# Kernel optimization log

Hardware: AMD Instinct MI355X
Metric: run time of the kernel (lower is better)

The kernel has to match this reference:

```python
import jax, jax.numpy as jnp
import numpy as np

N = 1_000_000
D_IN = 57   # hardcoded reshape(1,57) in original aggregate()
D_OUT = 128
K = 3       # num_sample=3 hardcoded in _get_unique_neighs_list


def _masked_mean_aggregate(h, neigh_idx, neigh_mask):
    # h: [N, D]; neigh_idx: [N, K] int; neigh_mask: [N, K] {0,1}
    feats = h[neigh_idx]                                   # [N, K, D] gather
    m = neigh_mask.astype(h.dtype)[..., None]              # [N, K, 1]
    s = jnp.sum(feats * m, axis=1)                         # [N, D]
    cnt = jnp.maximum(jnp.sum(neigh_mask, axis=1, keepdims=True).astype(h.dtype), 1.0)
    return s / cnt                                         # mask.mm(embed_matrix) equivalent (segment mean)


def _sage_layer(self_feats, aggregate_feats, W):
    # combined = cat([self, agg], dim=1); relu(W @ combined^T)^T; L2 normalize
    combined = jnp.concatenate([self_feats, aggregate_feats], axis=1)  # [N, 2D]
    out = jax.nn.relu(combined @ W.T)                                  # [N, out]
    norm = jnp.linalg.norm(out, axis=-1, keepdims=True)
    return out / jnp.maximum(norm, 1e-12)                              # F.normalize p=2 eps=1e-12


def setup_inputs() -> dict:
    key = jax.random.key(0)
    ks = jax.random.split(key, 7)
    x = jax.random.normal(ks[0], (N, D_IN), dtype=jnp.float32)
    W1 = jax.random.normal(ks[1], (D_OUT, 2 * D_IN), dtype=jnp.float32) * 0.1
    W2 = jax.random.normal(ks[2], (D_OUT, 2 * D_OUT), dtype=jnp.float32) * 0.1
    neigh_idx1 = jax.random.randint(ks[3], (N, K), 0, N, dtype=jnp.int32)
    neigh_mask1 = jax.random.randint(ks[4], (N, K), 0, 2, dtype=jnp.int32)
    neigh_idx2 = jax.random.randint(ks[5], (N, K), 0, N, dtype=jnp.int32)
    neigh_mask2 = jax.random.randint(ks[6], (N, K), 0, 2, dtype=jnp.int32)
    return {"x": x, "W1": W1, "W2": W2,
            "neigh_idx1": neigh_idx1, "neigh_mask1": neigh_mask1,
            "neigh_idx2": neigh_idx2, "neigh_mask2": neigh_mask2}


def reference(x, W1, W2, neigh_idx1, neigh_mask1, neigh_idx2, neigh_mask2):
    # Layer 1: aggregate over sampled neighbors of raw features, then SageLayer
    agg1 = _masked_mean_aggregate(x, neigh_idx1, neigh_mask1)
    h1 = _sage_layer(x, agg1, W1)                 # [N, D_OUT]
    # Layer 2
    agg2 = _masked_mean_aggregate(h1, neigh_idx2, neigh_mask2)
    h2 = _sage_layer(h1, agg2, W2)                # [N, D_OUT]
    return h2
```

## Files before the change

### kernel.cpp

```cpp
#include <hip/hip_runtime.h>
#include <hip/hip_bf16.h>

#define NN 1000000
#define NG 15625

typedef short bf16x8 __attribute__((ext_vector_type(8)));
typedef float f32x4  __attribute__((ext_vector_type(4)));
typedef unsigned short u16x8 __attribute__((ext_vector_type(8)));
typedef unsigned short u16x4 __attribute__((ext_vector_type(4)));

__device__ __forceinline__ float bf2f(unsigned short u){
  unsigned int x = ((unsigned int)u) << 16; float f;
  __builtin_memcpy(&f, &x, 4); return f;
}
__device__ __forceinline__ short f2bf(float v){
  __hip_bfloat16 h = __float2bfloat16(v); short s;
  __builtin_memcpy(&s, &h, 2); return s;
}

__global__ __launch_bounds__(256, 2) void sage2_mfma(
    const unsigned short* __restrict__ h1, const float* __restrict__ W2,
    const int* __restrict__ nidx, const int* __restrict__ nmask,
    float* __restrict__ out)
{
  __shared__ unsigned short comb[64 * 256];
  __shared__ float red[64][4];
  const int t   = threadIdx.x;
  const int l   = t & 63;
  const int w   = t >> 6;
  const int cfr = l & 15;
  const int kg  = l >> 4;

  bf16x8 Bf[8][2];
  #pragma unroll
  for (int ks = 0; ks < 8; ++ks) {
    #pragma unroll
    for (int nf = 0; nf < 2; ++nf) {
      const int col = w*32 + nf*16 + cfr;
      const int k0  = ks*32 + kg*8;
      const float* p = W2 + col*256 + k0;
      f32x4 a = *reinterpret_cast<const f32x4*>(p);
      f32x4 b = *reinterpret_cast<const f32x4*>(p + 4);
      bf16x8 v;
      v[0]=f2bf(a[0]); v[1]=f2bf(a[1]); v[2]=f2bf(a[2]); v[3]=f2bf(a[3]);
      v[4]=f2bf(b[0]); v[5]=f2bf(b[1]); v[6]=f2bf(b[2]); v[7]=f2bf(b[3]);
      Bf[ks][nf] = v;
    }
  }

  const u16x8* hp = reinterpret_cast<const u16x8*>(h1);
  char* cb = reinterpret_cast<char*>(comb);

  u16x8 sS[4], s0[4], s1[4], s2[4];
  float m0[4], m1[4], m2[4], iv[4];

  auto ISSUE = [&](int g){
    const long gb = (long)g * 64;
    #pragma unroll
    for (int i = 0; i < 4; ++i) {
      int it = t + i*256;
      int n = it >> 4, q = it & 15;
      long node = gb + n;
      int j0 = nidx[node*3+0], j1 = nidx[node*3+1], j2 = nidx[node*3+2];
      int b0 = nmask[node*3+0], b1 = nmask[node*3+1], b2 = nmask[node*3+2];
      m0[i]=(float)b0; m1[i]=(float)b1; m2[i]=(float)b2;
      int c = b0+b1+b2; iv[i] = 1.0f/(float)(c<1?1:c);
      u16x8 z = {};
      sS[i] = hp[node*16 + q];
      s0[i] = b0 ? hp[(long)j0*16 + q] : z;
      s1[i] = b1 ? hp[(long)j1*16 + q] : z;
      s2[i] = b2 ? hp[(long)j2*16 + q] : z;
    }
  };

  if (blockIdx.x < NG) ISSUE(blockIdx.x);

  for (int g = blockIdx.x; g < NG; g += gridDim.x) {
    const long gb = (long)g * 64;
    #pragma unroll
    for (int i = 0; i < 4; ++i) {
      int it = t + i*256;
      int n = it >> 4, q = it & 15;
      int sw = (n & 7) << 4;
      *reinterpret_cast<u16x8*>(cb + n*512 + ((q*16) ^ sw)) = sS[i];
      u16x8 r;
      #pragma unroll
      for (int j = 0; j < 8; ++j)
        r[j] = (unsigned short)f2bf(
            (m0[i]*bf2f(s0[i][j]) + m1[i]*bf2f(s1[i][j]) + m2[i]*bf2f(s2[i][j])) * iv[i]);
      *reinterpret_cast<u16x8*>(cb + n*512 + ((256 + q*16) ^ sw)) = r;
    }
    __syncthreads();

    int gn = g + gridDim.x;
    if (gn < NG) ISSUE(gn);

    f32x4 acc[4][2];
    #pragma unroll
    for (int r = 0; r < 4; ++r) {
      acc[r][0] = (f32x4){0.f,0.f,0.f,0.f};
      acc[r][1] = (f32x4){0.f,0.f,0.f,0.f};
    }
    const int sw = (cfr & 7) << 4;
    #pragma unroll
    for (int r = 0; r < 4; ++r) {
      const int rb = (r*16 + cfr) * 512;
      #pragma unroll
      for (int ks = 0; ks < 8; ++ks) {
        bf16x8 af = *reinterpret_cast<const bf16x8*>(cb + rb + ((ks*64 + kg*16) ^ sw));
        acc[r][0] = __builtin_amdgcn_mfma_f32_16x16x32_bf16(af, Bf[ks][0], acc[r][0], 0,0,0);
        acc[r][1] = __builtin_amdgcn_mfma_f32_16x16x32_bf16(af, Bf[ks][1], acc[r][1], 0,0,0);
      }
    }

    float ssv[4][4];
    #pragma unroll
    for (int r = 0; r < 4; ++r) {
      #pragma unroll
      for (int e = 0; e < 4; ++e) {
        float v0 = fmaxf(acc[r][0][e], 0.f); acc[r][0][e] = v0;
        float v1 = fmaxf(acc[r][1][e], 0.f); acc[r][1][e] = v1;
        float s = v0*v0 + v1*v1;
        s += __shfl_xor(s, 1); s += __shfl_xor(s, 2);
        s += __shfl_xor(s, 4); s += __shfl_xor(s, 8);
        ssv[r][e] = s;
      }
      if (cfr < 4) {
        float v = cfr==0 ? ssv[r][0] : cfr==1 ? ssv[r][1] : cfr==2 ? ssv[r][2] : ssv[r][3];
        red[r*16 + kg*4 + cfr][w] = v;
      }
    }
    __syncthreads();

    #pragma unroll
    for (int r = 0; r < 4; ++r) {
      #pragma unroll
      for (int e = 0; e < 4; ++e) {
        int row = r*16 + kg*4 + e;
        float tot = red[row][0] + red[row][1] + red[row][2] + red[row][3];
        float inv = 1.0f / fmaxf(sqrtf(tot), 1e-12f);
        long node = gb + row;
        out[node*128 + w*32 + cfr]      = acc[r][0][e] * inv;
        out[node*128 + w*32 + 16 + cfr] = acc[r][1][e] * inv;
      }
    }
  }
}

__global__ __launch_bounds__(256, 2) void sage1_mfma(
    const float* __restrict__ x, const float* __restrict__ W1,
    const int* __restrict__ nidx, const int* __restrict__ nmask,
    unsigned short* __restrict__ h1)
{
  __shared__ unsigned short comb[64 * 128];
  __shared__ float red[64][4];
  const int t   = threadIdx.x;
  const int l   = t & 63;
  const int w   = t >> 6;
  const int cfr = l & 15;
  const int kg  = l >> 4;

  bf16x8 Bf[4][2];
  #pragma unroll
  for (int ks = 0; ks < 4; ++ks) {
    #pragma unroll
    for (int nf = 0; nf < 2; ++nf) {
      const int col = w*32 + nf*16 + cfr;
      const int k0  = ks*32 + kg*8;
      bf16x8 v;
      #pragma unroll
      for (int j = 0; j < 8; ++j) {
        int lk = k0 + j;
        int wk = lk < 64 ? lk : lk - 7;
        bool valid = (lk < 57) || (lk >= 64 && lk < 121);
        v[j] = valid ? f2bf(W1[col*114 + wk]) : (short)0;
      }
      Bf[ks][nf] = v;
    }
  }

  char* cb = reinterpret_cast<char*>(comb);

  f32x4 sf[4], n0[4], n1[4], n2[4];
  float m0[4], m1[4], m2[4], iv[4];

  auto ISSUE = [&](int g){
    const long gb = (long)g * 64;
    #pragma unroll
    for (int i = 0; i < 4; ++i) {
      int it = t + i*256;
      int n = it >> 4, q = it & 15;
      long node = gb + n;
      int j0 = nidx[node*3+0], j1 = nidx[node*3+1], j2 = nidx[node*3+2];
      int b0 = nmask[node*3+0], b1 = nmask[node*3+1], b2 = nmask[node*3+2];
      m0[i]=(float)b0; m1[i]=(float)b1; m2[i]=(float)b2;
      int c = b0+b1+b2; iv[i] = 1.0f/(float)(c<1?1:c);
      #pragma unroll
      for (int jj = 0; jj < 4; ++jj) {
        int j = q*4 + jj;
        bool jv = j < 57;
        sf[i][jj] = jv            ? x[node*57 + j]       : 0.f;
        n0[i][jj] = (b0 && jv)    ? x[(long)j0*57 + j]   : 0.f;
        n1[i][jj] = (b1 && jv)    ? x[(long)j1*57 + j]   : 0.f;
        n2[i][jj] = (b2 && jv)    ? x[(long)j2*57 + j]   : 0.f;
      }
    }
  };

  if (blockIdx.x < NG) ISSUE(blockIdx.x);

  for (int g = blockIdx.x; g < NG; g += gridDim.x) {
    const long gb = (long)g * 64;
    #pragma unroll
    for (int i = 0; i < 4; ++i) {
      int it = t + i*256;
      int n = it >> 4, q = it & 15;
      int sw = (n & 7) << 4;
      u16x4 vs, va;
      #pragma unroll
      for (int jj = 0; jj < 4; ++jj) {
        vs[jj] = (unsigned short)f2bf(sf[i][jj]);
        va[jj] = (unsigned short)f2bf(
            (m0[i]*n0[i][jj] + m1[i]*n1[i][jj] + m2[i]*n2[i][jj]) * iv[i]);
      }
      *reinterpret_cast<u16x4*>(cb + n*256 + ((q*8) ^ sw))        = vs;
      *reinterpret_cast<u16x4*>(cb + n*256 + ((128 + q*8) ^ sw))  = va;
    }
    __syncthreads();

    int gn = g + gridDim.x;
    if (gn < NG) ISSUE(gn);

    f32x4 acc[4][2];
    #pragma unroll
    for (int r = 0; r < 4; ++r) {
      acc[r][0] = (f32x4){0.f,0.f,0.f,0.f};
      acc[r][1] = (f32x4){0.f,0.f,0.f,0.f};
    }
    const int sw = (cfr & 7) << 4;
    #pragma unroll
    for (int r = 0; r < 4; ++r) {
      const int rb = (r*16 + cfr) * 256;
      #pragma unroll
      for (int ks = 0; ks < 4; ++ks) {
        bf16x8 af = *reinterpret_cast<const bf16x8*>(cb + rb + ((ks*64 + kg*16) ^ sw));
        acc[r][0] = __builtin_amdgcn_mfma_f32_16x16x32_bf16(af, Bf[ks][0], acc[r][0], 0,0,0);
        acc[r][1] = __builtin_amdgcn_mfma_f32_16x16x32_bf16(af, Bf[ks][1], acc[r][1], 0,0,0);
      }
    }

    float ssv[4][4];
    #pragma unroll
    for (int r = 0; r < 4; ++r) {
      #pragma unroll
      for (int e = 0; e < 4; ++e) {
        float v0 = fmaxf(acc[r][0][e], 0.f); acc[r][0][e] = v0;
        float v1 = fmaxf(acc[r][1][e], 0.f); acc[r][1][e] = v1;
        float s = v0*v0 + v1*v1;
        s += __shfl_xor(s, 1); s += __shfl_xor(s, 2);
        s += __shfl_xor(s, 4); s += __shfl_xor(s, 8);
        ssv[r][e] = s;
      }
      if (cfr < 4) {
        float v = cfr==0 ? ssv[r][0] : cfr==1 ? ssv[r][1] : cfr==2 ? ssv[r][2] : ssv[r][3];
        red[r*16 + kg*4 + cfr][w] = v;
      }
    }
    __syncthreads();

    #pragma unroll
    for (int r = 0; r < 4; ++r) {
      #pragma unroll
      for (int e = 0; e < 4; ++e) {
        int row = r*16 + kg*4 + e;
        float tot = red[row][0] + red[row][1] + red[row][2] + red[row][3];
        float inv = 1.0f / fmaxf(sqrtf(tot), 1e-12f);
        long node = gb + row;
        h1[node*128 + w*32 + cfr]      = (unsigned short)f2bf(acc[r][0][e] * inv);
        h1[node*128 + w*32 + 16 + cfr] = (unsigned short)f2bf(acc[r][1][e] * inv);
      }
    }
  }
}

extern "C" void kernel_launch(void* const* d_in, const int* in_sizes, int n_in,
                              void* d_out, int out_size, void* d_ws, size_t ws_size,
                              hipStream_t stream) {
  const float* x   = (const float*)d_in[0];
  const float* W1  = (const float*)d_in[1];
  const float* W2  = (const float*)d_in[2];
  const int* idx1  = (const int*)d_in[3];
  const int* msk1  = (const int*)d_in[4];
  const int* idx2  = (const int*)d_in[5];
  const int* msk2  = (const int*)d_in[6];
  float* out = (float*)d_out;
  unsigned short* h1 = (unsigned short*)d_ws;

  sage1_mfma<<<2048, 256, 0, stream>>>(x, W1, idx1, msk1, h1);
  sage2_mfma<<<1024, 256, 0, stream>>>(h1, W2, idx2, msk2, out);
}
```

Baseline: 735.7 us.

## Use 512-thread blocks with double-buffered LDS and two-stage index/gather prefetch

```diff
diff --git a/kernel.cpp b/kernel.cpp
--- a/kernel.cpp
+++ b/kernel.cpp
@@ -3,6 +3,7 @@
 
 #define NN 1000000
 #define NG 15625
+#define GRID 1024
 
 typedef short bf16x8 __attribute__((ext_vector_type(8)));
 typedef float f32x4  __attribute__((ext_vector_type(4)));
@@ -18,68 +19,70 @@
   __builtin_memcpy(&s, &h, 2); return s;
 }
 
-__global__ __launch_bounds__(256, 2) void sage2_mfma(
+__global__ __launch_bounds__(512, 4) void sage2_mfma(
     const unsigned short* __restrict__ h1, const float* __restrict__ W2,
     const int* __restrict__ nidx, const int* __restrict__ nmask,
     float* __restrict__ out)
 {
-  __shared__ unsigned short comb[64 * 256];
-  __shared__ float red[64][4];
+  __shared__ unsigned short comb[2][64 * 256];
+  __shared__ float red[64][8];
   const int t   = threadIdx.x;
   const int l   = t & 63;
   const int w   = t >> 6;
   const int cfr = l & 15;
   const int kg  = l >> 4;
 
-  bf16x8 Bf[8][2];
+  bf16x8 Bf[8];
   #pragma unroll
   for (int ks = 0; ks < 8; ++ks) {
-    #pragma unroll
-    for (int nf = 0; nf < 2; ++nf) {
-      const int col = w*32 + nf*16 + cfr;
-      const int k0  = ks*32 + kg*8;
-      const float* p = W2 + col*256 + k0;
-      f32x4 a = *reinterpret_cast<const f32x4*>(p);
-      f32x4 b = *reinterpret_cast<const f32x4*>(p + 4);
-      bf16x8 v;
-      v[0]=f2bf(a[0]); v[1]=f2bf(a[1]); v[2]=f2bf(a[2]); v[3]=f2bf(a[3]);
-      v[4]=f2bf(b[0]); v[5]=f2bf(b[1]); v[6]=f2bf(b[2]); v[7]=f2bf(b[3]);
-      Bf[ks][nf] = v;
-    }
+    const int col = w*16 + cfr;
+    const int k0  = ks*32 + kg*8;
+    const float* p = W2 + col*256 + k0;
+    f32x4 a = *reinterpret_cast<const f32x4*>(p);
+    f32x4 b = *reinterpret_cast<const f32x4*>(p + 4);
+    bf16x8 v;
+    v[0]=f2bf(a[0]); v[1]=f2bf(a[1]); v[2]=f2bf(a[2]); v[3]=f2bf(a[3]);
+    v[4]=f2bf(b[0]); v[5]=f2bf(b[1]); v[6]=f2bf(b[2]); v[7]=f2bf(b[3]);
+    Bf[ks] = v;
   }
 
   const u16x8* hp = reinterpret_cast<const u16x8*>(h1);
-  char* cb = reinterpret_cast<char*>(comb);
-
-  u16x8 sS[4], s0[4], s1[4], s2[4];
-  float m0[4], m1[4], m2[4], iv[4];
-
-  auto ISSUE = [&](int g){
-    const long gb = (long)g * 64;
-    #pragma unroll
-    for (int i = 0; i < 4; ++i) {
-      int it = t + i*256;
+
+  int nib0[2], nib1[2], nib2[2], nmb0[2], nmb1[2], nmb2[2];
+  u16x8 sS[2], s0[2], s1[2], s2[2];
+  float m0[2], m1[2], m2[2], iv[2];
+
+  auto IDX = [&](int g){
+    const long gb = (long)g * 64;
+    #pragma unroll
+    for (int i = 0; i < 2; ++i) {
+      int n = (t + i*512) >> 4;
+      long node = gb + n;
+      nib0[i] = nidx[node*3+0]; nib1[i] = nidx[node*3+1]; nib2[i] = nidx[node*3+2];
+      nmb0[i] = nmask[node*3+0]; nmb1[i] = nmask[node*3+1]; nmb2[i] = nmask[node*3+2];
+    }
+  };
+  auto GATHER = [&](int g){
+    const long gb = (long)g * 64;
+    #pragma unroll
+    for (int i = 0; i < 2; ++i) {
+      int it = t + i*512;
       int n = it >> 4, q = it & 15;
       long node = gb + n;
-      int j0 = nidx[node*3+0], j1 = nidx[node*3+1], j2 = nidx[node*3+2];
-      int b0 = nmask[node*3+0], b1 = nmask[node*3+1], b2 = nmask[node*3+2];
+      int b0 = nmb0[i], b1 = nmb1[i], b2 = nmb2[i];
       m0[i]=(float)b0; m1[i]=(float)b1; m2[i]=(float)b2;
       int c = b0+b1+b2; iv[i] = 1.0f/(float)(c<1?1:c);
-      u16x8 z = {};
       sS[i] = hp[node*16 + q];
-      s0[i] = b0 ? hp[(long)j0*16 + q] : z;
-      s1[i] = b1 ? hp[(long)j1*16 + q] : z;
-      s2[i] = b2 ? hp[(long)j2*16 + q] : z;
-    }
-  };
-
-  if (blockIdx.x < NG) ISSUE(blockIdx.x);
-
-  for (int g = blockIdx.x; g < NG; g += gridDim.x) {
-    const long gb = (long)g * 64;
-    #pragma unroll
-    for (int i = 0; i < 4; ++i) {
-      int it = t + i*256;
+      s0[i] = hp[(long)nib0[i]*16 + q];
+      s1[i] = hp[(long)nib1[i]*16 + q];
+      s2[i] = hp[(long)nib2[i]*16 + q];
+    }
+  };
+  auto UNPACK = [&](int p){
+    char* cb = reinterpret_cast<char*>(comb[p]);
+    #pragma unroll
+    for (int i = 0; i < 2; ++i) {
+      int it = t + i*512;
       int n = it >> 4, q = it & 15;
       int sw = (n & 7) << 4;
       *reinterpret_cast<u16x8*>(cb + n*512 + ((q*16) ^ sw)) = sS[i];
@@ -90,26 +93,34 @@
             (m0[i]*bf2f(s0[i][j]) + m1[i]*bf2f(s1[i][j]) + m2[i]*bf2f(s2[i][j])) * iv[i]);
       *reinterpret_cast<u16x8*>(cb + n*512 + ((256 + q*16) ^ sw)) = r;
     }
+  };
+
+  const int g0 = blockIdx.x;
+  IDX(g0); GATHER(g0);
+  if (g0 + (int)gridDim.x < NG) IDX(g0 + gridDim.x);
+
+  int p = 0;
+  for (int g = g0; g < NG; g += gridDim.x) {
+    const long gb = (long)g * 64;
+    UNPACK(p);
     __syncthreads();
 
-    int gn = g + gridDim.x;
-    if (gn < NG) ISSUE(gn);
-
-    f32x4 acc[4][2];
-    #pragma unroll
-    for (int r = 0; r < 4; ++r) {
-      acc[r][0] = (f32x4){0.f,0.f,0.f,0.f};
-      acc[r][1] = (f32x4){0.f,0.f,0.f,0.f};
-    }
-    const int sw = (cfr & 7) << 4;
+    int g1 = g + gridDim.x, g2 = g + 2*gridDim.x;
+    if (g1 < NG) GATHER(g1);
+    if (g2 < NG) IDX(g2);
+
+    f32x4 acc[4];
+    #pragma unroll
+    for (int r = 0; r < 4; ++r) acc[r] = (f32x4){0.f,0.f,0.f,0.f};
+    const int swz = (cfr & 7) << 4;
+    char* cbp = reinterpret_cast<char*>(comb[p]);
     #pragma unroll
     for (int r = 0; r < 4; ++r) {
       const int rb = (r*16 + cfr) * 512;
       #pragma unroll
       for (int ks = 0; ks < 8; ++ks) {
-        bf16x8 af = *reinterpret_cast<const bf16x8*>(cb + rb + ((ks*64 + kg*16) ^ sw));
-        acc[r][0] = __builtin_amdgcn_mfma_f32_16x16x32_bf16(af, Bf[ks][0], acc[r][0], 0,0,0);
-        acc[r][1] = __builtin_amdgcn_mfma_f32_16x16x32_bf16(af, Bf[ks][1], acc[r][1], 0,0,0);
+        bf16x8 af = *reinterpret_cast<const bf16x8*>(cbp + rb + ((ks*64 + kg*16) ^ swz));
+        acc[r] = __builtin_amdgcn_mfma_f32_16x16x32_bf16(af, Bf[ks], acc[r], 0,0,0);
       }
     }
 
@@ -118,9 +129,8 @@
     for (int r = 0; r < 4; ++r) {
       #pragma unroll
       for (int e = 0; e < 4; ++e) {
-        float v0 = fmaxf(acc[r][0][e], 0.f); acc[r][0][e] = v0;
-        float v1 = fmaxf(acc[r][1][e], 0.f); acc[r][1][e] = v1;
-        float s = v0*v0 + v1*v1;
+        float v = fmaxf(acc[r][e], 0.f); acc[r][e] = v;
+        float s = v*v;
         s += __shfl_xor(s, 1); s += __shfl_xor(s, 2);
         s += __shfl_xor(s, 4); s += __shfl_xor(s, 8);
         ssv[r][e] = s;
@@ -137,83 +147,85 @@
       #pragma unroll
       for (int e = 0; e < 4; ++e) {
         int row = r*16 + kg*4 + e;
-        float tot = red[row][0] + red[row][1] + red[row][2] + red[row][3];
+        f32x4 ra = *reinterpret_cast<const f32x4*>(&red[row][0]);
+        f32x4 rb = *reinterpret_cast<const f32x4*>(&red[row][4]);
+        float tot = (ra[0]+ra[1]) + (ra[2]+ra[3]) + (rb[0]+rb[1]) + (rb[2]+rb[3]);
         float inv = 1.0f / fmaxf(sqrtf(tot), 1e-12f);
-        long node = gb + row;
-        out[node*128 + w*32 + cfr]      = acc[r][0][e] * inv;
-        out[node*128 + w*32 + 16 + cfr] = acc[r][1][e] * inv;
-      }
-    }
+        out[(gb + row)*128 + w*16 + cfr] = acc[r][e] * inv;
+      }
+    }
+    p ^= 1;
   }
 }
 
-__global__ __launch_bounds__(256, 2) void sage1_mfma(
+__global__ __launch_bounds__(512, 4) void sage1_mfma(
     const float* __restrict__ x, const float* __restrict__ W1,
     const int* __restrict__ nidx, const int* __restrict__ nmask,
     unsigned short* __restrict__ h1)
 {
-  __shared__ unsigned short comb[64 * 128];
-  __shared__ float red[64][4];
+  __shared__ unsigned short comb[2][64 * 128];
+  __shared__ float red[64][8];
   const int t   = threadIdx.x;
   const int l   = t & 63;
   const int w   = t >> 6;
   const int cfr = l & 15;
   const int kg  = l >> 4;
 
-  bf16x8 Bf[4][2];
+  bf16x8 Bf[4];
   #pragma unroll
   for (int ks = 0; ks < 4; ++ks) {
-    #pragma unroll
-    for (int nf = 0; nf < 2; ++nf) {
-      const int col = w*32 + nf*16 + cfr;
-      const int k0  = ks*32 + kg*8;
-      bf16x8 v;
-      #pragma unroll
-      for (int j = 0; j < 8; ++j) {
-        int lk = k0 + j;
-        int wk = lk < 64 ? lk : lk - 7;
-        bool valid = (lk < 57) || (lk >= 64 && lk < 121);
-        v[j] = valid ? f2bf(W1[col*114 + wk]) : (short)0;
-      }
-      Bf[ks][nf] = v;
-    }
+    const int col = w*16 + cfr;
+    const int k0  = ks*32 + kg*8;
+    bf16x8 v;
+    #pragma unroll
+    for (int j = 0; j < 8; ++j) {
+      int lk = k0 + j;
+      int wk = lk < 64 ? lk : lk - 7;
+      bool valid = (lk < 57) || (lk >= 64 && lk < 121);
+      v[j] = valid ? f2bf(W1[col*114 + wk]) : (short)0;
+    }
+    Bf[ks] = v;
   }
 
-  char* cb = reinterpret_cast<char*>(comb);
-
-  f32x4 sf[4], n0[4], n1[4], n2[4];
-  float m0[4], m1[4], m2[4], iv[4];
-
-  auto ISSUE = [&](int g){
-    const long gb = (long)g * 64;
-    #pragma unroll
-    for (int i = 0; i < 4; ++i) {
-      int it = t + i*256;
+  int nib0[2], nib1[2], nib2[2], nmb0[2], nmb1[2], nmb2[2];
+  f32x4 sf[2], n0[2], n1[2], n2[2];
+  float m0[2], m1[2], m2[2], iv[2];
+
+  auto IDX = [&](int g){
+    const long gb = (long)g * 64;
+    #pragma unroll
+    for (int i = 0; i < 2; ++i) {
+      int n = (t + i*512) >> 4;
+      long node = gb + n;
+      nib0[i] = nidx[node*3+0]; nib1[i] = nidx[node*3+1]; nib2[i] = nidx[node*3+2];
+      nmb0[i] = nmask[node*3+0]; nmb1[i] = nmask[node*3+1]; nmb2[i] = nmask[node*3+2];
+    }
+  };
+  auto GATHER = [&](int g){
+    const long gb = (long)g * 64;
+    #pragma unroll
+    for (int i = 0; i < 2; ++i) {
+      int it = t + i*512;
       int n = it >> 4, q = it & 15;
       long node = gb + n;
-      int j0 = nidx[node*3+0], j1 = nidx[node*3+1], j2 = nidx[node*3+2];
-      int b0 = nmask[node*3+0], b1 = nmask[node*3+1], b2 = nmask[node*3+2];
+      int b0 = nmb0[i], b1 = nmb1[i], b2 = nmb2[i];
       m0[i]=(float)b0; m1[i]=(float)b1; m2[i]=(float)b2;
       int c = b0+b1+b2; iv[i] = 1.0f/(float)(c<1?1:c);
       #pragma unroll
       for (int jj = 0; jj < 4; ++jj) {
-        int j = q*4 + jj;
-        bool jv = j < 57;
-        sf[i][jj] = jv            ? x[node*57 + j]       : 0.f;
-        n0[i][jj] = (b0 && jv)    ? x[(long)j0*57 + j]   : 0.f;
-        n1[i][jj] = (b1 && jv)    ? x[(long)j1*57 + j]   : 0.f;
-        n2[i][jj] = (b2 && jv)    ? x[(long)j2*57 + j]   : 0.f;
-      }
-    }
-  };
-
-  if (blockIdx.x < NG) ISSUE(blockIdx.x);
-
-  for (int g = blockIdx.x; g < NG; g += gridDim.x) {
-    const long gb = (long)g * 64;
-    #pragma unroll
-    for (int i = 0; i < 4; ++i) {
-      int it = t + i*256;
+        int j = q*4 + jj; int jc = j < 57 ? j : 56;
+        sf[i][jj] = x[node*57 + jc];
+        n0[i][jj] = x[(long)nib0[i]*57 + jc];
+        n1[i][jj] = x[(long)nib1[i]*57 + jc];
+        n2[i][jj] = x[(long)nib2[i]*57 + jc];
+      }
+    }
+  };
+  auto UNPACK = [&](int p){
+    char* cb = reinterpret_cast<char*>(comb[p]);
+    #pragma unroll
+    for (int i = 0; i < 2; ++i) {
+      int it = t + i*512;
       int n = it >> 4, q = it & 15;
       int sw = (n & 7) << 4;
       u16x4 vs, va;
@@ -223,29 +235,37 @@
         va[jj] = (unsigned short)f2bf(
             (m0[i]*n0[i][jj] + m1[i]*n1[i][jj] + m2[i]*n2[i][jj]) * iv[i]);
       }
-      *reinterpret_cast<u16x4*>(cb + n*256 + ((q*8) ^ sw))        = vs;
-      *reinterpret_cast<u16x4*>(cb + n*256 + ((128 + q*8) ^ sw))  = va;
-    }
+      *reinterpret_cast<u16x4*>(cb + n*256 + ((q*8) ^ sw))       = vs;
+      *reinterpret_cast<u16x4*>(cb + n*256 + ((128 + q*8) ^ sw)) = va;
+    }
+  };
+
+  const int g0 = blockIdx.x;
+  IDX(g0); GATHER(g0);
+  if (g0 + (int)gridDim.x < NG) IDX(g0 + gridDim.x);
+
+  int p = 0;
+  for (int g = g0; g < NG; g += gridDim.x) {
+    const long gb = (long)g * 64;
+    UNPACK(p);
     __syncthreads();
 
-    int gn = g + gridDim.x;
-    if (gn < NG) ISSUE(gn);
-
-    f32x4 acc[4][2];
-    #pragma unroll
-    for (int r = 0; r < 4; ++r) {
-      acc[r][0] = (f32x4){0.f,0.f,0.f,0.f};
-      acc[r][1] = (f32x4){0.f,0.f,0.f,0.f};
-    }
-    const int sw = (cfr & 7) << 4;
+    int g1 = g + gridDim.x, g2 = g + 2*gridDim.x;
+    if (g1 < NG) GATHER(g1);
+    if (g2 < NG) IDX(g2);
+
+    f32x4 acc[4];
+    #pragma unroll
+    for (int r = 0; r < 4; ++r) acc[r] = (f32x4){0.f,0.f,0.f,0.f};
+    const int swz = (cfr & 7) << 4;
+    char* cbp = reinterpret_cast<char*>(comb[p]);
     #pragma unroll
     for (int r = 0; r < 4; ++r) {
       const int rb = (r*16 + cfr) * 256;
       #pragma unroll
       for (int ks = 0; ks < 4; ++ks) {
-        bf16x8 af = *reinterpret_cast<const bf16x8*>(cb + rb + ((ks*64 + kg*16) ^ sw));
-        acc[r][0] = __builtin_amdgcn_mfma_f32_16x16x32_bf16(af, Bf[ks][0], acc[r][0], 0,0,0);
-        acc[r][1] = __builtin_amdgcn_mfma_f32_16x16x32_bf16(af, Bf[ks][1], acc[r][1], 0,0,0);
+        bf16x8 af = *reinterpret_cast<const bf16x8*>(cbp + rb + ((ks*64 + kg*16) ^ swz));
+        acc[r] = __builtin_amdgcn_mfma_f32_16x16x32_bf16(af, Bf[ks], acc[r], 0,0,0);
       }
     }
 
@@ -254,9 +274,8 @@
     for (int r = 0; r < 4; ++r) {
       #pragma unroll
       for (int e = 0; e < 4; ++e) {
-        float v0 = fmaxf(acc[r][0][e], 0.f); acc[r][0][e] = v0;
-        float v1 = fmaxf(acc[r][1][e], 0.f); acc[r][1][e] = v1;
-        float s = v0*v0 + v1*v1;
+        float v = fmaxf(acc[r][e], 0.f); acc[r][e] = v;
+        float s = v*v;
         s += __shfl_xor(s, 1); s += __shfl_xor(s, 2);
         s += __shfl_xor(s, 4); s += __shfl_xor(s, 8);
         ssv[r][e] = s;
@@ -273,13 +292,14 @@
       #pragma unroll
       for (int e = 0; e < 4; ++e) {
         int row = r*16 + kg*4 + e;
-        float tot = red[row][0] + red[row][1] + red[row][2] + red[row][3];
+        f32x4 ra = *reinterpret_cast<const f32x4*>(&red[row][0]);
+        f32x4 rb = *reinterpret_cast<const f32x4*>(&red[row][4]);
+        float tot = (ra[0]+ra[1]) + (ra[2]+ra[3]) + (rb[0]+rb[1]) + (rb[2]+rb[3]);
         float inv = 1.0f / fmaxf(sqrtf(tot), 1e-12f);
-        long node = gb + row;
-        h1[node*128 + w*32 + cfr]      = (unsigned short)f2bf(acc[r][0][e] * inv);
-        h1[node*128 + w*32 + 16 + cfr] = (unsigned short)f2bf(acc[r][1][e] * inv);
-      }
-    }
+        h1[(gb + row)*128 + w*16 + cfr] = (unsigned short)f2bf(acc[r][e] * inv);
+      }
+    }
+    p ^= 1;
   }
 }
 
@@ -296,6 +316,6 @@
   float* out = (float*)d_out;
   unsigned short* h1 = (unsigned short*)d_ws;
 
-  sage1_mfma<<<2048, 256, 0, stream>>>(x, W1, idx1, msk1, h1);
-  sage2_mfma<<<1024, 256, 0, stream>>>(h1, W2, idx2, msk2, out);
-}
+  sage1_mfma<<<GRID, 512, 0, stream>>>(x, W1, idx1, msk1, h1);
+  sage2_mfma<<<GRID, 512, 0, stream>>>(h1, W2, idx2, msk2, out);
+}
```

After: 1.350 ms. 83.5% more time.
